# Performance work log

Measured on AMD Instinct MI355X. Metric: run time of the kernel, lower is better.

The kernel has to match this reference:

```python
import jax, jax.numpy as jnp
import numpy as np
import math

EMB_S = 64
HEADS = 8
EMB = EMB_S * HEADS  # 512
M = int(EMB_S * 0.5)  # 32 random features
B, T = 8, 4096
EPS = 1e-5


def setup_inputs() -> dict:
    key = jax.random.key(0)
    ks = jax.random.split(key, 16)
    s_in = 1.0 / math.sqrt(EMB_S)
    s_emb = 1.0 / math.sqrt(EMB)
    s_hid = 1.0 / math.sqrt(4 * EMB)
    return {
        "x": jax.random.normal(ks[0], (B, T, EMB), jnp.float32),
        "w": jax.random.normal(ks[1], (M, EMB_S), jnp.float32),  # frozen random features
        "kqv_w": jax.random.uniform(ks[2], (3 * EMB_S, EMB_S), jnp.float32, -s_in, s_in),
        "kqv_b": jax.random.uniform(ks[3], (3 * EMB_S,), jnp.float32, -s_in, s_in),
        "proj_w": jax.random.uniform(ks[4], (EMB, EMB), jnp.float32, -s_emb, s_emb),
        "proj_b": jax.random.uniform(ks[5], (EMB,), jnp.float32, -s_emb, s_emb),
        "ln1_g": 1.0 + 0.02 * jax.random.normal(ks[6], (EMB,), jnp.float32),
        "ln1_b": 0.02 * jax.random.normal(ks[7], (EMB,), jnp.float32),
        "ln2_g": 1.0 + 0.02 * jax.random.normal(ks[8], (EMB,), jnp.float32),
        "ln2_b": 0.02 * jax.random.normal(ks[9], (EMB,), jnp.float32),
        "mlp_w1": jax.random.uniform(ks[10], (4 * EMB, EMB), jnp.float32, -s_emb, s_emb),
        "mlp_b1": jax.random.uniform(ks[11], (4 * EMB,), jnp.float32, -s_emb, s_emb),
        "mlp_w2": jax.random.uniform(ks[12], (EMB, 4 * EMB), jnp.float32, -s_hid, s_hid),
        "mlp_b2": jax.random.uniform(ks[13], (EMB,), jnp.float32, -s_hid, s_hid),
    }


def _layer_norm(x, g, b):
    mu = jnp.mean(x, axis=-1, keepdims=True)
    var = jnp.mean(jnp.square(x - mu), axis=-1, keepdims=True)
    return (x - mu) * jax.lax.rsqrt(var + EPS) * g + b


def _prm_exp(z, w):
    # z: [B,T,H,E]; softmax-kernel random features, [B,T,H,M]
    xd = 0.5 * jnp.sum(z * z, axis=-1, keepdims=True)
    wtx = jnp.einsum("bthe,me->bthm", z, w)
    return jnp.exp(wtx - xd) / math.sqrt(M)


def reference(x, w, kqv_w, kqv_b, proj_w, proj_b, ln1_g, ln1_b, ln2_g, ln2_b,
              mlp_w1, mlp_b1, mlp_w2, mlp_b2):
    Bb, Tt, _ = x.shape
    h = _layer_norm(x, ln1_g, ln1_b).reshape(Bb, Tt, HEADS, EMB_S)
    kqv = jnp.einsum("bthe,fe->bthf", h, kqv_w) + kqv_b  # [B,T,H,3E]
    k, q, v = jnp.split(kqv, 3, axis=-1)  # torch.split order: k, q, v
    kp = _prm_exp(k, w)  # [B,T,H,M]
    qp = _prm_exp(q, w)
    D = jnp.einsum("bthm,bhm->bth", qp, kp.sum(axis=1))  # [B,T,H]
    kptv = jnp.einsum("bthe,bthm->bhem", v, kp)  # [B,H,E,M]
    y = jnp.einsum("bthm,bhem->bthe", qp, kptv) / D[..., None]
    y = y.reshape(Bb, Tt, EMB)
    attn = jnp.einsum("btf,ef->bte", y, proj_w) + proj_b  # dropout = identity (eval)
    x = x + attn
    h2 = _layer_norm(x, ln2_g, ln2_b)
    hid = jax.nn.gelu(jnp.einsum("bte,fe->btf", h2, mlp_w1) + mlp_b1, approximate=False)
    mlp_out = jnp.einsum("btf,ef->bte", hid, mlp_w2) + mlp_b2
    return x + mlp_out
```

## Files before the change

### kernel.cpp

```cpp
#include <hip/hip_runtime.h>
#include <hip/hip_bf16.h>

typedef __bf16 bf16x8_t __attribute__((ext_vector_type(8)));
typedef float f32x4_t __attribute__((ext_vector_type(4)));
using bf16 = __hip_bfloat16;

#define EMB 512
#define NTOK 32768
#define NROW 262144
#define SQRT_M_INV 0.17677669529663687f
#define KNC 16

__device__ __forceinline__ void gload16(const void* g, void* l) {
  __builtin_amdgcn_global_load_lds((const __attribute__((address_space(1))) void*)g,
                                   (__attribute__((address_space(3))) void*)l, 16, 0, 0);
}

__device__ __forceinline__ float fast_gelu(float v) {
  float u = v * 0.70710678118654752f;
  float a = fabsf(u);
  float tt = __builtin_amdgcn_rcpf(fmaf(0.3275911f, a, 1.0f));
  float p = fmaf(tt, 1.061405429f, -1.453152027f);
  p = fmaf(tt, p, 1.421413741f);
  p = fmaf(tt, p, -0.284496736f);
  p = fmaf(tt, p, 0.254829592f);
  p = p * tt;
  float e = __expf(-a * a);
  float er = fmaf(-p, e, 1.0f);
  er = copysignf(er, u);
  return 0.5f * v * (1.0f + er);
}

__device__ __forceinline__ void cvt4(const float* __restrict__ in,
                                     bf16* __restrict__ out, int i4, int n4) {
  if (i4 < n4) {
    float4 v = ((const float4*)in)[i4];
    alignas(8) bf16 o[4];
    o[0] = __float2bfloat16(v.x); o[1] = __float2bfloat16(v.y);
    o[2] = __float2bfloat16(v.z); o[3] = __float2bfloat16(v.w);
    *(uint2*)(out + i4 * 4) = *(const uint2*)o;
  }
}
__global__ __launch_bounds__(256) void f2b4_kernel(
    const float* __restrict__ a, bf16* __restrict__ oa, int na4,
    const float* __restrict__ b, bf16* __restrict__ ob, int nb4,
    const float* __restrict__ c, bf16* __restrict__ oc, int nc4,
    const float* __restrict__ d, bf16* __restrict__ od, int nd4) {
  int i4 = blockIdx.x * 256 + threadIdx.x;
  cvt4(a, oa, i4, na4);
  cvt4(b, ob, i4, nb4);
  cvt4(c, oc, i4, nc4);
  cvt4(d, od, i4, nd4);
}

__global__ __launch_bounds__(256) void ln_kernel(const float* __restrict__ x,
                                                 const float* __restrict__ g,
                                                 const float* __restrict__ bt,
                                                 bf16* __restrict__ out) {
  int lane = threadIdx.x & 63;
  int row = blockIdx.x * 4 + (threadIdx.x >> 6);
  const float* xr = x + (size_t)row * EMB;
  float4 v0 = ((const float4*)xr)[lane * 2];
  float4 v1 = ((const float4*)xr)[lane * 2 + 1];
  float s = v0.x + v0.y + v0.z + v0.w + v1.x + v1.y + v1.z + v1.w;
#pragma unroll
  for (int o = 32; o; o >>= 1) s += __shfl_xor(s, o);
  float mu = s * (1.0f / 512.0f);
  float vs = 0.f, d;
  d = v0.x - mu; vs += d * d;  d = v0.y - mu; vs += d * d;
  d = v0.z - mu; vs += d * d;  d = v0.w - mu; vs += d * d;
  d = v1.x - mu; vs += d * d;  d = v1.y - mu; vs += d * d;
  d = v1.z - mu; vs += d * d;  d = v1.w - mu; vs += d * d;
#pragma unroll
  for (int o = 32; o; o >>= 1) vs += __shfl_xor(vs, o);
  float rstd = rsqrtf(vs * (1.0f / 512.0f) + 1e-5f);
  float4 g0 = ((const float4*)g)[lane * 2], g1 = ((const float4*)g)[lane * 2 + 1];
  float4 b0 = ((const float4*)bt)[lane * 2], b1 = ((const float4*)bt)[lane * 2 + 1];
  alignas(16) bf16 o8[8];
  o8[0] = __float2bfloat16((v0.x - mu) * rstd * g0.x + b0.x);
  o8[1] = __float2bfloat16((v0.y - mu) * rstd * g0.y + b0.y);
  o8[2] = __float2bfloat16((v0.z - mu) * rstd * g0.z + b0.z);
  o8[3] = __float2bfloat16((v0.w - mu) * rstd * g0.w + b0.w);
  o8[4] = __float2bfloat16((v1.x - mu) * rstd * g1.x + b1.x);
  o8[5] = __float2bfloat16((v1.y - mu) * rstd * g1.y + b1.y);
  o8[6] = __float2bfloat16((v1.z - mu) * rstd * g1.z + b1.z);
  o8[7] = __float2bfloat16((v1.w - mu) * rstd * g1.w + b1.w);
  *(uint4*)(out + (size_t)row * EMB + lane * 8) = *(const uint4*)o8;
}

template <int BM, int BN, int WM, int WN, int OP>
__global__ __launch_bounds__(256) void gemm_bt(const bf16* __restrict__ A,
                                               const bf16* __restrict__ W,
                                               const float* __restrict__ bias,
                                               const float* __restrict__ res,
                                               float* __restrict__ outF,
                                               bf16* __restrict__ outB,
                                               int M, int N, int K) {
  constexpr int BK = 32;
  constexpr int TM = BM / WM, TN = BN / WN;
  constexpr int NI = TM / 16, NJ = TN / 16;
  constexpr int AP = BM * BK / 2048;
  constexpr int WP = BN * BK / 2048;
  alignas(16) __shared__ bf16 As[2][BM * BK];
  alignas(16) __shared__ bf16 Ws[2][BN * BK];
  int t = threadIdx.x;
  int lane = t & 63, wid = t >> 6;
  int wm = wid % WM, wn = wid / WM;
  int nwg = gridDim.x * gridDim.y;
  int lin = blockIdx.y * gridDim.x + blockIdx.x;
  if ((nwg & 7) == 0) lin = (lin & 7) * (nwg >> 3) + (lin >> 3);
  int bn = (lin % gridDim.x) * BN, bm = (lin / gridDim.x) * BM;
  int lr = lane & 15, lq = lane >> 4;
  const int r0 = (t * 8) >> 5, c0 = (t * 8) & 31;

  const bf16* ap = A + (size_t)(bm + r0) * K + c0;
  const bf16* wp = W + (size_t)(bn + r0) * K + c0;
  const size_t strA = (size_t)64 * K;

  f32x4_t acc[NI][NJ];
#pragma unroll
  for (int i = 0; i < NI; ++i)
#pragma unroll
    for (int j = 0; j < NJ; ++j)
#pragma unroll
      for (int r = 0; r < 4; ++r) acc[i][j][r] = 0.f;

  auto stage = [&](int buf) {
#pragma unroll
    for (int p = 0; p < AP; ++p)
      gload16(ap + (size_t)p * strA, &As[buf][(r0 + p * 64) * BK + c0]);
#pragma unroll
    for (int p = 0; p < WP; ++p)
      gload16(wp + (size_t)p * strA, &Ws[buf][(r0 + p * 64) * BK + c0]);
    ap += BK;
    wp += BK;
  };
  auto compute = [&](int buf) {
    bf16x8_t afr[NI], bfr[NJ];
#pragma unroll
    for (int i = 0; i < NI; ++i)
      afr[i] = *(const bf16x8_t*)&As[buf][(wm * TM + i * 16 + lr) * BK + lq * 8];
#pragma unroll
    for (int j = 0; j < NJ; ++j)
      bfr[j] = *(const bf16x8_t*)&Ws[buf][(wn * TN + j * 16 + lr) * BK + lq * 8];
#pragma unroll
    for (int i = 0; i < NI; ++i)
#pragma unroll
      for (int j = 0; j < NJ; ++j)
        acc[i][j] = __builtin_amdgcn_mfma_f32_16x16x32_bf16(afr[i], bfr[j], acc[i][j], 0, 0, 0);
  };

  const int nt = K / BK;
  stage(0);
  int cur = 0;
  for (int kt = 0; kt < nt - 1; ++kt) {
    __syncthreads();
    stage(cur ^ 1);
    compute(cur);
    cur ^= 1;
  }
  __syncthreads();
  compute(cur);

#pragma unroll
  for (int i = 0; i < NI; ++i)
#pragma unroll
    for (int j = 0; j < NJ; ++j) {
      int gn = bn + wn * TN + j * 16 + lr;
      float bv = bias[gn];
#pragma unroll
      for (int r = 0; r < 4; ++r) {
        int gm = bm + wm * TM + i * 16 + lq * 4 + r;
        float v = acc[i][j][r] + bv;
        size_t off = (size_t)gm * N + gn;
        if (OP == 0) {
          outF[off] = v;
        } else if (OP == 1) {
          outF[off] = v + res[off];
        } else {
          outB[off] = __float2bfloat16(fast_gelu(v));
        }
      }
    }
}

__device__ __forceinline__ size_t bh_row(size_t grow) {
  size_t h = grow & 7, bt = grow >> 3;
  size_t b = bt >> 12, tt = bt & 4095;
  return ((b * 8 + h) << 12) + tt;
}

__global__ __launch_bounds__(256) void kqv_prm_kernel(
    const bf16* __restrict__ A,
    const bf16* __restrict__ Wk,
    const float* __restrict__ bias,
    const float* __restrict__ wrf,
    float* __restrict__ kp, float* __restrict__ qp,
    bf16* __restrict__ vout) {
  constexpr int LDZ = 136;
  constexpr int LDV = 72;
  alignas(16) __shared__ char u_raw[27648];
  bf16* As  = (bf16*)u_raw;
  bf16* Ws  = (bf16*)(u_raw + 4096);
  bf16* zkq = (bf16*)u_raw;
  bf16* vs  = (bf16*)(u_raw + 17408);
  float* xd_s = (float*)(u_raw + 26624);

  int t = threadIdx.x;
  int lane = t & 63, wid = t >> 6;
  int wm = wid & 1, wn = wid >> 1;
  int lr = lane & 15, lq = lane >> 4;
  size_t row0 = (size_t)blockIdx.x * 64;

  bf16x8_t wfrag[2][2];
#pragma unroll
  for (int mt = 0; mt < 2; ++mt)
#pragma unroll
    for (int ks = 0; ks < 2; ++ks) {
      const float* src = wrf + (mt * 16 + lr) * 64 + ks * 32 + lq * 8;
#pragma unroll
      for (int jj = 0; jj < 8; ++jj) wfrag[mt][ks][jj] = (__bf16)src[jj];
    }

  f32x4_t acc[2][6];
#pragma unroll
  for (int i = 0; i < 2; ++i)
#pragma unroll
    for (int j = 0; j < 6; ++j)
#pragma unroll
      for (int r = 0; r < 4; ++r) acc[i][j][r] = 0.f;

  const int r0 = t >> 2, c0 = (t * 8) & 31;
  for (int k0 = 0; k0 < 64; k0 += 32) {
    gload16(&A[(row0 + r0) * 64 + k0 + c0], &As[r0 * 32 + c0]);
#pragma unroll
    for (int p = 0; p < 3; ++p) {
      int r = r0 + p * 64;
      gload16(&Wk[(size_t)r * 64 + k0 + c0], &Ws[r * 32 + c0]);
    }
    __syncthreads();
    bf16x8_t af[2], bfr[6];
#pragma unroll
    for (int i = 0; i < 2; ++i)
      af[i] = *(const bf16x8_t*)&As[(wm * 32 + i * 16 + lr) * 32 + lq * 8];
#pragma unroll
    for (int j = 0; j < 6; ++j)
      bfr[j] = *(const bf16x8_t*)&Ws[(wn * 96 + j * 16 + lr) * 32 + lq * 8];
#pragma unroll
    for (int i = 0; i < 2; ++i)
#pragma unroll
      for (int j = 0; j < 6; ++j)
        acc[i][j] = __builtin_amdgcn_mfma_f32_16x16x32_bf16(af[i], bfr[j], acc[i][j], 0, 0, 0);
    __syncthreads();
  }

#pragma unroll
  for (int i = 0; i < 2; ++i)
#pragma unroll
    for (int j = 0; j < 6; ++j) {
      int col = wn * 96 + j * 16 + lr;
      float bv = bias[col];
      int rowb = wm * 32 + i * 16 + lq * 4;
#pragma unroll
      for (int r = 0; r < 4; ++r) {
        float v = acc[i][j][r] + bv;
        if (col < 128) zkq[(rowb + r) * LDZ + col] = __float2bfloat16(v);
        else           vs[(rowb + r) * LDV + (col - 128)] = __float2bfloat16(v);
      }
    }
  __syncthreads();

  if (t < 128) {
    int r = t & 63, sel = t >> 6;
    const bf16* zr = &zkq[r * LDZ + sel * 64];
    float xd = 0.f;
#pragma unroll
    for (int c = 0; c < 64; c += 8) {
      bf16x8_t z8 = *(const bf16x8_t*)&zr[c];
#pragma unroll
      for (int jj = 0; jj < 8; ++jj) { float f = (float)z8[jj]; xd += f * f; }
    }
    xd_s[r * 2 + sel] = 0.5f * xd;
  }
  __syncthreads();

#pragma unroll
  for (int p = 0; p < 2; ++p) {
    int idx = t + p * 256;
    int r = idx >> 3, c8 = idx & 7;
    size_t nr = bh_row(row0 + r);
    *(uint4*)&vout[nr * 64 + c8 * 8] = *(const uint4*)&vs[r * LDV + c8 * 8];
  }

  int sel = wn;
  f32x4_t aw[2][2];
#pragma unroll
  for (int i = 0; i < 2; ++i)
#pragma unroll
    for (int mt = 0; mt < 2; ++mt)
#pragma unroll
      for (int r = 0; r < 4; ++r) aw[i][mt][r] = 0.f;
#pragma unroll
  for (int ks = 0; ks < 2; ++ks) {
    bf16x8_t af2[2];
#pragma unroll
    for (int i = 0; i < 2; ++i)
      af2[i] = *(const bf16x8_t*)&zkq[(wm * 32 + i * 16 + lr) * LDZ + sel * 64 + ks * 32 + lq * 8];
#pragma unroll
    for (int i = 0; i < 2; ++i)
#pragma unroll
      for (int mt = 0; mt < 2; ++mt)
        aw[i][mt] = __builtin_amdgcn_mfma_f32_16x16x32_bf16(af2[i], wfrag[mt][ks], aw[i][mt], 0, 0, 0);
  }
  float* outp = sel ? qp : kp;
#pragma unroll
  for (int i = 0; i < 2; ++i)
#pragma unroll
    for (int r = 0; r < 4; ++r) {
      int row = wm * 32 + i * 16 + lq * 4 + r;
      size_t nr = bh_row(row0 + row);
#pragma unroll
      for (int mt = 0; mt < 2; ++mt) {
        int m = mt * 16 + lr;
        outp[nr * 32 + m] =
            __expf(aw[i][mt][r] - xd_s[row * 2 + sel]) * SQRT_M_INV;
      }
    }
}

__global__ __launch_bounds__(256) void kptv_kernel(const bf16* __restrict__ v2,
                                                   const float* __restrict__ kp2,
                                                   float* __restrict__ part) {
  int bh = blockIdx.x, chunk = blockIdx.y;
  int t = threadIdx.x;
  int ts = t >> 6;
  int eg = (t >> 2) & 15;
  int g  = t & 3;
  const int T0 = chunk * 256;
  const bf16* vp = v2 + ((size_t)bh * 4096 + T0) * 64 + eg * 4;
  const float* kpp = kp2 + ((size_t)bh * 4096 + T0) * 32 + g * 8;

  float acc[4][8];
  float accs[8];
#pragma unroll
  for (int e = 0; e < 4; ++e)
#pragma unroll
    for (int m = 0; m < 8; ++m) acc[e][m] = 0.f;
#pragma unroll
  for (int m = 0; m < 8; ++m) accs[m] = 0.f;

#pragma unroll 2
  for (int tok = ts; tok < 256; tok += 4) {
    union { uint2 u; ushort s[4]; } vr;
    vr.u = *(const uint2*)(vp + (size_t)tok * 64);
    float ve[4];
#pragma unroll
    for (int e = 0; e < 4; ++e)
      ve[e] = __uint_as_float((uint32_t)vr.s[e] << 16);
    float4 k0 = *(const float4*)(kpp + (size_t)tok * 32);
    float4 k1 = *(const float4*)(kpp + (size_t)tok * 32 + 4);
    float km[8] = {k0.x, k0.y, k0.z, k0.w, k1.x, k1.y, k1.z, k1.w};
#pragma unroll
    for (int e = 0; e < 4; ++e)
#pragma unroll
      for (int m = 0; m < 8; ++m) acc[e][m] = fmaf(ve[e], km[m], acc[e][m]);
#pragma unroll
    for (int m = 0; m < 8; ++m) accs[m] += km[m];
  }

  __shared__ float red[256][33];
  __shared__ float reds[4][4][8];
#pragma unroll
  for (int e = 0; e < 4; ++e)
#pragma unroll
    for (int m = 0; m < 8; ++m) red[t][e * 8 + m] = acc[e][m];
  if (eg == 0) {
#pragma unroll
    for (int m = 0; m < 8; ++m) reds[ts][g][m] = accs[m];
  }
  __syncthreads();

  int l = t >> 2, q = t & 3;
  int leg = l >> 2, lg = l & 3;
  float o[8];
#pragma unroll
  for (int m = 0; m < 8; ++m)
    o[m] = red[l][q * 8 + m] + red[l + 64][q * 8 + m] +
           red[l + 128][q * 8 + m] + red[l + 192][q * 8 + m];
  float* pp = part + (size_t)(bh * KNC + chunk) * 2080 + (leg * 4 + q) * 32 + lg * 8;
  *(float4*)pp = make_float4(o[0], o[1], o[2], o[3]);
  *(float4*)(pp + 4) = make_float4(o[4], o[5], o[6], o[7]);
  if (t < 32) {
    int g2 = t >> 3, j = t & 7;
    float s = reds[0][g2][j] + reds[1][g2][j] + reds[2][g2][j] + reds[3][g2][j];
    part[(size_t)(bh * KNC + chunk) * 2080 + 2048 + g2 * 8 + j] = s;
  }
}

__global__ __launch_bounds__(256) void y_kernel(const float* __restrict__ qp2,
                                                const float* __restrict__ part,
                                                bf16* __restrict__ y) {
  int bh = blockIdx.x, chunk = blockIdx.y;
  int b = bh >> 3, h = bh & 7;
  __shared__ float kv_s[64][36];
  __shared__ float ks_s[32];
  __shared__ float inv_dd[512];
  alignas(16) __shared__ float qp_s[2][16][32];
  int t = threadIdx.x;
  int e = t & 63, iq = t >> 6;
  const int T0 = chunk * 512;
  const size_t qbase = (size_t)bh * 4096 + T0;

  {
    int er = t >> 2, m0 = (t & 3) * 8;
    float4 a0 = make_float4(0.f, 0.f, 0.f, 0.f);
    float4 a1 = make_float4(0.f, 0.f, 0.f, 0.f);
#pragma unroll 4
    for (int c = 0; c < KNC; ++c) {
      const float* pp = part + (size_t)(bh * KNC + c) * 2080 + er * 32 + m0;
      float4 u = *(const float4*)pp;
      float4 v = *(const float4*)(pp + 4);
      a0.x += u.x; a0.y += u.y; a0.z += u.z; a0.w += u.w;
      a1.x += v.x; a1.y += v.y; a1.z += v.z; a1.w += v.w;
    }
    *(float4*)&kv_s[er][m0] = a0;
    *(float4*)&kv_s[er][m0 + 4] = a1;
    if (t < 32) {
      float s = 0.f;
#pragma unroll 4
      for (int c = 0; c < KNC; ++c)
        s += part[(size_t)(bh * KNC + c) * 2080 + 2048 + t];
      ks_s[t] = s;
    }
  }
  __syncthreads();

  float kv[32];
#pragma unroll
  for (int m = 0; m < 32; m += 4) *(float4*)&kv[m] = *(const float4*)&kv_s[e][m];

  if (t < 128)
    gload16(qp2 + (qbase + (t >> 3)) * 32 + (t & 7) * 4,
            &qp_s[0][t >> 3][(t & 7) * 4]);

  {
    float ks[32];
#pragma unroll
    for (int m = 0; m < 32; m += 4) *(float4*)&ks[m] = *(const float4*)&ks_s[m];
#pragma unroll
    for (int p = 0; p < 2; ++p) {
      int tok = t + p * 256;
      const float* qrow = qp2 + (qbase + tok) * 32;
      float dd = 0.f;
#pragma unroll
      for (int m = 0; m < 32; m += 4) {
        float4 qq = *(const float4*)&qrow[m];
        dd += qq.x * ks[m] + qq.y * ks[m + 1] + qq.z * ks[m + 2] + qq.w * ks[m + 3];
      }
      inv_dd[tok] = 1.0f / dd;
    }
  }

  float dreg[4];
  int cur = 0;
  for (int grp = 0; grp < 32; ++grp) {
    __syncthreads();
    if (grp > 0) {
      int tokp = (grp - 1) * 16 + iq * 4;
#pragma unroll
      for (int i0 = 0; i0 < 4; ++i0)
        y[(size_t)(b * 4096 + T0 + tokp + i0) * EMB + h * 64 + e] =
            __float2bfloat16(dreg[i0]);
    }
    if (grp < 31 && t < 128) {
      int nr = (grp + 1) * 16;
      gload16(qp2 + (qbase + nr + (t >> 3)) * 32 + (t & 7) * 4,
              &qp_s[cur ^ 1][t >> 3][(t & 7) * 4]);
    }
#pragma unroll
    for (int i0 = 0; i0 < 4; ++i0) {
      int i = iq * 4 + i0;
      float dot = 0.f;
#pragma unroll
      for (int m = 0; m < 32; m += 4) {
        float4 qq = *(const float4*)&qp_s[cur][i][m];
        dot += qq.x * kv[m] + qq.y * kv[m + 1] + qq.z * kv[m + 2] + qq.w * kv[m + 3];
      }
      dreg[i0] = dot * inv_dd[grp * 16 + i];
    }
    cur ^= 1;
  }
#pragma unroll
  for (int i0 = 0; i0 < 4; ++i0) {
    int tokp = 31 * 16 + iq * 4 + i0;
    y[(size_t)(b * 4096 + T0 + tokp) * EMB + h * 64 + e] =
        __float2bfloat16(dreg[i0]);
  }
}

extern "C" void kernel_launch(void* const* d_in, const int* in_sizes, int n_in,
                              void* d_out, int out_size, void* d_ws, size_t ws_size,
                              hipStream_t stream) {
  const float* x      = (const float*)d_in[0];
  const float* w      = (const float*)d_in[1];
  const float* kqv_w  = (const float*)d_in[2];
  const float* kqv_b  = (const float*)d_in[3];
  const float* proj_w = (const float*)d_in[4];
  const float* proj_b = (const float*)d_in[5];
  const float* ln1_g  = (const float*)d_in[6];
  const float* ln1_b  = (const float*)d_in[7];
  const float* ln2_g  = (const float*)d_in[8];
  const float* ln2_b  = (const float*)d_in[9];
  const float* mlp_w1 = (const float*)d_in[10];
  const float* mlp_b1 = (const float*)d_in[11];
  const float* mlp_w2 = (const float*)d_in[12];
  const float* mlp_b2 = (const float*)d_in[13];
  float* out = (float*)d_out;

  char* ws = (char*)d_ws;
  size_t off = 0;
  auto alloc = [&](size_t bytes) -> void* {
    void* p = ws + off;
    off = (off + bytes + 255) & ~(size_t)255;
    return p;
  };

  bf16* kqv_wb  = (bf16*)alloc(12288 * 2);
  bf16* proj_wb = (bf16*)alloc(262144 * 2);
  bf16* w1b     = (bf16*)alloc(1048576 * 2);
  bf16* w2b     = (bf16*)alloc(1048576 * 2);
  bf16* hb      = (bf16*)alloc((size_t)NTOK * EMB * 2);
  bf16* yb      = hb;
  float* qpb    = (float*)alloc((size_t)NROW * 32 * 4);
  bf16* h2b     = (bf16*)qpb;
  float* kpb    = (float*)alloc((size_t)NROW * 32 * 4);
  bf16* hidb    = (bf16*)kpb;
  bf16* vb      = (bf16*)alloc((size_t)NROW * 64 * 2);
  float* partb  = (float*)alloc((size_t)64 * KNC * 2080 * 4);

  f2b4_kernel<<<1024, 256, 0, stream>>>(kqv_w, kqv_wb, 12288 / 4,
                                        proj_w, proj_wb, 262144 / 4,
                                        mlp_w1, w1b, 1048576 / 4,
                                        mlp_w2, w2b, 1048576 / 4);

  ln_kernel<<<NTOK / 4, 256, 0, stream>>>(x, ln1_g, ln1_b, hb);

  kqv_prm_kernel<<<NROW / 64, 256, 0, stream>>>(hb, kqv_wb, kqv_b, w, kpb, qpb, vb);

  kptv_kernel<<<dim3(64, KNC), 256, 0, stream>>>(vb, kpb, partb);

  y_kernel<<<dim3(64, 8), 256, 0, stream>>>(qpb, partb, yb);

  gemm_bt<128, 128, 2, 2, 1><<<dim3(4, NTOK / 128), 256, 0, stream>>>(
      yb, proj_wb, proj_b, x, out, nullptr, NTOK, 512, 512);

  ln_kernel<<<NTOK / 4, 256, 0, stream>>>(out, ln2_g, ln2_b, h2b);

  for (int c = 0; c < 2; ++c) {
    const bf16* h2c = h2b + (size_t)c * 16384 * 512;
    float* outc = out + (size_t)c * 16384 * 512;
    gemm_bt<128, 128, 2, 2, 2><<<dim3(16, 128), 256, 0, stream>>>(
        h2c, w1b, mlp_b1, nullptr, nullptr, hidb, 16384, 2048, 512);
    gemm_bt<64, 128, 1, 4, 1><<<dim3(4, 256), 256, 0, stream>>>(
        hidb, w2b, mlp_b2, outc, outc, nullptr, 16384, 512, 2048);
  }
}
```

Before: 578.7 us.

## Triple-buffer GEMM LDS staging with partial vmcnt waits and XOR swizzle

The bf16 GEMM moves from double-buffered to triple-buffered LDS staging. Each iteration waits only until the oldest tile's global-to-LDS loads finish (partial vmcnt) instead of a full syncthreads drain, so two tiles stay in flight during compute. It also adds an XOR swizzle on the LDS column chunk, applied through the global source address and the fragment reads, to cut bank conflicts. The cost is 1.5x the LDS per block, which may lower occupancy, plus explicit waitcnt/barrier code whose correctness depends on load counting.

```diff
diff --git a/kernel.cpp b/kernel.cpp
--- a/kernel.cpp
+++ b/kernel.cpp
@@ -14,6 +14,11 @@
 __device__ __forceinline__ void gload16(const void* g, void* l) {
   __builtin_amdgcn_global_load_lds((const __attribute__((address_space(1))) void*)g,
                                    (__attribute__((address_space(3))) void*)l, 16, 0, 0);
+}
+
+template <int N> __device__ __forceinline__ void wait_vm_lgkm0() {
+  asm volatile("s_waitcnt vmcnt(%0) lgkmcnt(0)" :: "n"(N) : "memory");
+  __builtin_amdgcn_sched_barrier(0);
 }
 
 __device__ __forceinline__ float fast_gelu(float v) {
@@ -101,8 +106,9 @@
   constexpr int NI = TM / 16, NJ = TN / 16;
   constexpr int AP = BM * BK / 2048;
   constexpr int WP = BN * BK / 2048;
-  alignas(16) __shared__ bf16 As[2][BM * BK];
-  alignas(16) __shared__ bf16 Ws[2][BN * BK];
+  constexpr int LPT = AP + WP;
+  alignas(16) __shared__ bf16 As[3][BM * BK];
+  alignas(16) __shared__ bf16 Ws[3][BN * BK];
   int t = threadIdx.x;
   int lane = t & 63, wid = t >> 6;
   int wm = wid % WM, wn = wid / WM;
@@ -111,10 +117,15 @@
   if ((nwg & 7) == 0) lin = (lin & 7) * (nwg >> 3) + (lin >> 3);
   int bn = (lin % gridDim.x) * BN, bm = (lin / gridDim.x) * BM;
   int lr = lane & 15, lq = lane >> 4;
-  const int r0 = (t * 8) >> 5, c0 = (t * 8) & 31;
-
-  const bf16* ap = A + (size_t)(bm + r0) * K + c0;
-  const bf16* wp = W + (size_t)(bn + r0) * K + c0;
+
+  const int r0 = t >> 2;
+  const int c0lin = (t & 3) * 8;
+  const int sc = (r0 >> 1) & 3;
+  const int c0g = ((t & 3) ^ sc) * 8;
+  const int rsw = (lq ^ ((lr >> 1) & 3)) * 8;
+
+  const bf16* ap = A + (size_t)(bm + r0) * K + c0g;
+  const bf16* wp = W + (size_t)(bn + r0) * K + c0g;
   const size_t strA = (size_t)64 * K;
 
   f32x4_t acc[NI][NJ];
@@ -128,10 +139,10 @@
   auto stage = [&](int buf) {
 #pragma unroll
     for (int p = 0; p < AP; ++p)
-      gload16(ap + (size_t)p * strA, &As[buf][(r0 + p * 64) * BK + c0]);
+      gload16(ap + (size_t)p * strA, &As[buf][(r0 + p * 64) * BK + c0lin]);
 #pragma unroll
     for (int p = 0; p < WP; ++p)
-      gload16(wp + (size_t)p * strA, &Ws[buf][(r0 + p * 64) * BK + c0]);
+      gload16(wp + (size_t)p * strA, &Ws[buf][(r0 + p * 64) * BK + c0lin]);
     ap += BK;
     wp += BK;
   };
@@ -139,10 +150,10 @@
     bf16x8_t afr[NI], bfr[NJ];
 #pragma unroll
     for (int i = 0; i < NI; ++i)
-      afr[i] = *(const bf16x8_t*)&As[buf][(wm * TM + i * 16 + lr) * BK + lq * 8];
+      afr[i] = *(const bf16x8_t*)&As[buf][(wm * TM + i * 16 + lr) * BK + rsw];
 #pragma unroll
     for (int j = 0; j < NJ; ++j)
-      bfr[j] = *(const bf16x8_t*)&Ws[buf][(wn * TN + j * 16 + lr) * BK + lq * 8];
+      bfr[j] = *(const bf16x8_t*)&Ws[buf][(wn * TN + j * 16 + lr) * BK + rsw];
 #pragma unroll
     for (int i = 0; i < NI; ++i)
 #pragma unroll
@@ -152,15 +163,26 @@
 
   const int nt = K / BK;
   stage(0);
-  int cur = 0;
-  for (int kt = 0; kt < nt - 1; ++kt) {
-    __syncthreads();
-    stage(cur ^ 1);
-    compute(cur);
-    cur ^= 1;
-  }
-  __syncthreads();
-  compute(cur);
+  stage(1);
+  int bc = 0, bs = 2;
+  for (int kt = 0; kt < nt - 2; ++kt) {
+    wait_vm_lgkm0<LPT>();
+    __builtin_amdgcn_s_barrier();
+    __builtin_amdgcn_sched_barrier(0);
+    stage(bs);
+    compute(bc);
+    bc = (bc == 2) ? 0 : bc + 1;
+    bs = (bs == 2) ? 0 : bs + 1;
+  }
+  wait_vm_lgkm0<LPT>();
+  __builtin_amdgcn_s_barrier();
+  __builtin_amdgcn_sched_barrier(0);
+  compute(bc);
+  bc = (bc == 2) ? 0 : bc + 1;
+  wait_vm_lgkm0<0>();
+  __builtin_amdgcn_s_barrier();
+  __builtin_amdgcn_sched_barrier(0);
+  compute(bc);
 
 #pragma unroll
   for (int i = 0; i < NI; ++i)
```

After: 550.6 us. 4.8% less time.
